# Optimization experiments

Hardware: AMD Instinct MI355X
Metric: run time of the kernel (lower is better)

## Reference

```python
import jax, jax.numpy as jnp
import numpy as np

B, S, D, H = 4, 4096, 1024, 128

def setup_inputs() -> dict:
    key = jax.random.key(0)
    ks = jax.random.split(key, 4)
    scale = 1.0 / np.sqrt(D)
    return {
        "x":  jax.random.normal(ks[0], (B, S, D), dtype=jnp.float32),
        "Wq": jax.random.normal(ks[1], (D, H), dtype=jnp.float32) * scale,
        "bq": jnp.zeros((H,), dtype=jnp.float32),
        "Wk": jax.random.normal(ks[2], (D, H), dtype=jnp.float32) * scale,
        "bk": jnp.zeros((H,), dtype=jnp.float32),
        "Wv": jax.random.normal(ks[3], (D, H), dtype=jnp.float32) * scale,
        "bv": jnp.zeros((H,), dtype=jnp.float32),
    }

def reference(x, Wq, bq, Wk, bk, Wv, bv):
    # q, k, v: [B, S, H]
    q = x @ Wq + bq
    k = x @ Wk + bk
    v = x @ Wv + bv
    inv_sqrt_h = 1.0 / jnp.sqrt(jnp.asarray(q.shape[-1], q.dtype))
    # scores: [B, S, S]
    scores = jnp.einsum('bqh,bkh->bqk', q, k) * inv_sqrt_h
    seq = q.shape[1]
    causal = jnp.tril(jnp.ones((seq, seq), dtype=bool))
    scores = jnp.where(causal, scores, jnp.asarray(-jnp.inf, scores.dtype))
    probs = jax.nn.softmax(scores, axis=-1)
    # dropout p=0.0 -> identity
    return jnp.einsum('bqk,bkh->bqh', probs, v)
```

## Files before the change

### kernel.cpp

```cpp
#include <hip/hip_runtime.h>
#include <hip/hip_bf16.h>

#define B_ 4
#define S_ 4096
#define D_ 1024
#define H_ 128

typedef _Float16 half8 __attribute__((ext_vector_type(8)));
typedef _Float16 half4v __attribute__((ext_vector_type(4)));
typedef float float4v __attribute__((ext_vector_type(4)));


__global__ __launch_bounds__(256) void k_cvt_w(const float* __restrict__ Wq,
                                               const float* __restrict__ Wk,
                                               const float* __restrict__ Wv,
                                               _Float16* __restrict__ WT) {
    const float* W = blockIdx.y == 0 ? Wq : (blockIdx.y == 1 ? Wk : Wv);
    int idx = blockIdx.x * 256 + threadIdx.x;
    int k = idx >> 7, n = idx & 127;
    WT[(size_t)blockIdx.y * (H_ * D_) + (size_t)n * D_ + k] = (_Float16)W[idx];
}

__global__ __launch_bounds__(256, 3) void k_proj(const float* __restrict__ X,
                                                 const _Float16* __restrict__ WT,
                                                 const float* __restrict__ bq,
                                                 const float* __restrict__ bk,
                                                 const float* __restrict__ bv,
                                                 _Float16* __restrict__ Qf,
                                                 _Float16* __restrict__ Kz,
                                                 _Float16* __restrict__ Vz) {
    __shared__ _Float16 smem[(64 + 128) * 72];
    _Float16* As = smem;
    _Float16* Bs = smem + 64 * 72;

    const int t    = threadIdx.x;
    const int bid  = blockIdx.x;
    const int w    = bid >> 8;
    const int m0   = (bid & 255) * 64;
    const int lane = t & 63, wid = t >> 6;
    const int lo   = lane & 15, hi = lane >> 4;
    const int wr   = wid >> 1, wc = wid & 1;

    const _Float16* Wt = WT + (size_t)w * (H_ * D_);

    const int ar = t >> 2, ac = (t & 3) * 16;
    const int br = t >> 1, bc = (t & 1) * 32;

    float4v acc[2][4];
#pragma unroll
    for (int mt = 0; mt < 2; ++mt)
#pragma unroll
        for (int nt = 0; nt < 4; ++nt) acc[mt][nt] = {0.f, 0.f, 0.f, 0.f};

    for (int it = 0; it < 16; ++it) {
        const int k0 = it * 64;
        __syncthreads();
        {
            const float* xp = X + (size_t)(m0 + ar) * D_ + k0 + ac;
            float4v x0 = *(const float4v*)(xp);
            float4v x1 = *(const float4v*)(xp + 4);
            float4v x2 = *(const float4v*)(xp + 8);
            float4v x3 = *(const float4v*)(xp + 12);
            half8 h0, h1;
            h0[0]=(_Float16)x0[0]; h0[1]=(_Float16)x0[1]; h0[2]=(_Float16)x0[2]; h0[3]=(_Float16)x0[3];
            h0[4]=(_Float16)x1[0]; h0[5]=(_Float16)x1[1]; h0[6]=(_Float16)x1[2]; h0[7]=(_Float16)x1[3];
            h1[0]=(_Float16)x2[0]; h1[1]=(_Float16)x2[1]; h1[2]=(_Float16)x2[2]; h1[3]=(_Float16)x2[3];
            h1[4]=(_Float16)x3[0]; h1[5]=(_Float16)x3[1]; h1[6]=(_Float16)x3[2]; h1[7]=(_Float16)x3[3];
            *(half8*)(&As[ar * 72 + ac])     = h0;
            *(half8*)(&As[ar * 72 + ac + 8]) = h1;
        }
        {
            const _Float16* wp = Wt + (size_t)br * D_ + k0 + bc;
            half8 b0 = *(const half8*)(wp);
            half8 b1 = *(const half8*)(wp + 8);
            half8 b2 = *(const half8*)(wp + 16);
            half8 b3 = *(const half8*)(wp + 24);
            *(half8*)(&Bs[br * 72 + bc])      = b0;
            *(half8*)(&Bs[br * 72 + bc + 8])  = b1;
            *(half8*)(&Bs[br * 72 + bc + 16]) = b2;
            *(half8*)(&Bs[br * 72 + bc + 24]) = b3;
        }
        __syncthreads();
#pragma unroll
        for (int kk = 0; kk < 2; ++kk) {
            half8 af[2], bf[4];
#pragma unroll
            for (int mt = 0; mt < 2; ++mt)
                af[mt] = *(const half8*)(&As[(wr * 32 + mt * 16 + lo) * 72 + kk * 32 + hi * 8]);
#pragma unroll
            for (int nt = 0; nt < 4; ++nt)
                bf[nt] = *(const half8*)(&Bs[(wc * 64 + nt * 16 + lo) * 72 + kk * 32 + hi * 8]);
#pragma unroll
            for (int mt = 0; mt < 2; ++mt)
#pragma unroll
                for (int nt = 0; nt < 4; ++nt)
                    acc[mt][nt] = __builtin_amdgcn_mfma_f32_16x16x32_f16(
                        af[mt], bf[nt], acc[mt][nt], 0, 0, 0);
        }
    }

    const float* bias = (w == 0) ? bq : ((w == 1) ? bk : bv);
    const float scale = (w == 0) ? (0.08838834764831845f * 1.4426950408889634f) : 1.0f;
    __syncthreads();
    _Float16* Ct = smem;
#pragma unroll
    for (int mt = 0; mt < 2; ++mt)
#pragma unroll
        for (int nt = 0; nt < 4; ++nt) {
            const int col   = wc * 64 + nt * 16 + lo;
            const float bn  = bias[col];
            const int rbase = wr * 32 + mt * 16 + 4 * hi;
#pragma unroll
            for (int j = 0; j < 4; ++j)
                Ct[(rbase + j) * 136 + col] = (_Float16)((acc[mt][nt][j] + bn) * scale);
        }
    __syncthreads();

    const int bb  = m0 >> 12;
    const int tt0 = (m0 & (S_ - 1)) >> 5;

    if (w == 0) {
        const int r = t >> 2, c0 = (t & 3) * 32;
        _Float16* dst = Qf + (size_t)(m0 + r) * H_ + c0;
        const _Float16* srcp = &Ct[r * 136 + c0];
#pragma unroll
        for (int cc = 0; cc < 4; ++cc)
            *(half8*)(dst + cc * 8) = *(const half8*)(srcp + cc * 8);
    } else if (w == 1) {
        const int rowp = ((lo >> 2) << 3) + (lo & 3);
#pragma unroll
        for (int q = 0; q < 4; ++q) {
            const int fid = wid * 4 + q;
            const int ft = fid >> 3, k2 = (fid >> 1) & 3, c = fid & 1;
            const int row = ft * 32 + rowp + 4 * c;
            half8 v = *(const half8*)(&Ct[row * 136 + k2 * 32 + hi * 8]);
            *(half8*)(Kz + (size_t)(bb * 128 + tt0 + ft) * 4096 +
                      (k2 * 2 + c) * 512 + lane * 8) = v;
        }
    } else {
#pragma unroll
        for (int q = 0; q < 4; ++q) {
            const int fid = wid * 4 + q;
            const int ft = fid >> 3, hc = fid & 7;
            half8 v;
#pragma unroll
            for (int e = 0; e < 8; ++e)
                v[e] = Ct[(ft * 32 + hi * 8 + e) * 136 + hc * 16 + lo];
            *(half8*)(Vz + (size_t)(bb * 128 + tt0 + ft) * 4096 +
                      hc * 512 + lane * 8) = v;
        }
    }
}

__global__ __launch_bounds__(512, 2) void k_attn(const _Float16* __restrict__ Qf,
                                                 const _Float16* __restrict__ Kz,
                                                 const _Float16* __restrict__ Vz,
                                                 float* __restrict__ Out) {
    __shared__ float    sm_l[8][32];
    __shared__ _Float16 sm_o[8][32][136];

    const int t    = threadIdx.x;
    const int lane = t & 63, wid = t >> 6;
    const int lo = lane & 15, hi = lane >> 4;

    const int i   = blockIdx.x;
    const int b   = (i >> 1) & 3;
    const int qtr = ((i >> 3) << 1) | (i & 1);
    const int qt  = (qtr < 64) ? qtr : (191 - qtr);
    const int q0  = qt << 5;

    const _Float16* Qb = Qf + (size_t)b * (S_ * H_);
    const _Float16* Kb = Kz + (size_t)b * 524288;
    const _Float16* Vb = Vz + (size_t)b * 524288;

    half8 qfa[4], qfb[4];
#pragma unroll
    for (int kk = 0; kk < 4; ++kk) {
        qfa[kk] = *(const half8*)(Qb + (size_t)(q0 + lo) * H_ + kk * 32 + hi * 8);
        qfb[kk] = *(const half8*)(Qb + (size_t)(q0 + 16 + lo) * H_ + kk * 32 + hi * 8);
    }

    float4v oa[8], ob[8];
#pragma unroll
    for (int hc = 0; hc < 8; ++hc) { oa[hc] = {0.f,0.f,0.f,0.f}; ob[hc] = {0.f,0.f,0.f,0.f}; }
    float la = 0.f, lb = 0.f;

    const int lane8 = lane * 8;
    const int ntiles = qt + 1;

    half8 kc0[4], kc1[4];
    if (wid < ntiles) {
        const _Float16* Kt = Kb + (size_t)wid * 4096 + lane8;
#pragma unroll
        for (int kk = 0; kk < 4; ++kk) {
            kc0[kk] = *(const half8*)(Kt + (kk * 2    ) * 512);
            kc1[kk] = *(const half8*)(Kt + (kk * 2 + 1) * 512);
        }
    }

    for (int tt = wid; tt < ntiles; tt += 8) {
        const _Float16* Vt = Vb + (size_t)tt * 4096 + lane8;
        half8 vf[8];
#pragma unroll
        for (int hc = 0; hc < 8; ++hc)
            vf[hc] = *(const half8*)(Vt + hc * 512);
        const int tn = (tt + 8 < ntiles) ? (tt + 8) : tt;
        half8 kn0[4], kn1[4];
        {
            const _Float16* Ktn = Kb + (size_t)tn * 4096 + lane8;
#pragma unroll
            for (int kk = 0; kk < 4; ++kk) {
                kn0[kk] = *(const half8*)(Ktn + (kk * 2    ) * 512);
                kn1[kk] = *(const half8*)(Ktn + (kk * 2 + 1) * 512);
            }
        }
        float4v s0a = {0.f,0.f,0.f,0.f}, s1a = {0.f,0.f,0.f,0.f};
        float4v s0b = {0.f,0.f,0.f,0.f}, s1b = {0.f,0.f,0.f,0.f};
#pragma unroll
        for (int kk = 0; kk < 4; ++kk) {
            s0a = __builtin_amdgcn_mfma_f32_16x16x32_f16(kc0[kk], qfa[kk], s0a, 0, 0, 0);
            s0b = __builtin_amdgcn_mfma_f32_16x16x32_f16(kc0[kk], qfb[kk], s0b, 0, 0, 0);
            s1a = __builtin_amdgcn_mfma_f32_16x16x32_f16(kc1[kk], qfa[kk], s1a, 0, 0, 0);
            s1b = __builtin_amdgcn_mfma_f32_16x16x32_f16(kc1[kk], qfb[kk], s1b, 0, 0, 0);
        }
        if (tt == qt) {
#pragma unroll
            for (int j = 0; j < 4; ++j) {
                const int c0 = 8 * hi + j, c1 = 8 * hi + 4 + j;
                if (c0 > lo)      s0a[j] = -INFINITY;
                if (c1 > lo)      s1a[j] = -INFINITY;
                if (c0 > 16 + lo) s0b[j] = -INFINITY;
                if (c1 > 16 + lo) s1b[j] = -INFINITY;
            }
        }
        float pa0 = __builtin_amdgcn_exp2f(s0a[0]), pa1 = __builtin_amdgcn_exp2f(s0a[1]);
        float pa2 = __builtin_amdgcn_exp2f(s0a[2]), pa3 = __builtin_amdgcn_exp2f(s0a[3]);
        float pa4 = __builtin_amdgcn_exp2f(s1a[0]), pa5 = __builtin_amdgcn_exp2f(s1a[1]);
        float pa6 = __builtin_amdgcn_exp2f(s1a[2]), pa7 = __builtin_amdgcn_exp2f(s1a[3]);
        float pb0 = __builtin_amdgcn_exp2f(s0b[0]), pb1 = __builtin_amdgcn_exp2f(s0b[1]);
        float pb2 = __builtin_amdgcn_exp2f(s0b[2]), pb3 = __builtin_amdgcn_exp2f(s0b[3]);
        float pb4 = __builtin_amdgcn_exp2f(s1b[0]), pb5 = __builtin_amdgcn_exp2f(s1b[1]);
        float pb6 = __builtin_amdgcn_exp2f(s1b[2]), pb7 = __builtin_amdgcn_exp2f(s1b[3]);
        la += ((pa0+pa1)+(pa2+pa3)) + ((pa4+pa5)+(pa6+pa7));
        lb += ((pb0+pb1)+(pb2+pb3)) + ((pb4+pb5)+(pb6+pb7));
        half8 pfa, pfb;
        pfa[0]=(_Float16)pa0; pfa[1]=(_Float16)pa1; pfa[2]=(_Float16)pa2; pfa[3]=(_Float16)pa3;
        pfa[4]=(_Float16)pa4; pfa[5]=(_Float16)pa5; pfa[6]=(_Float16)pa6; pfa[7]=(_Float16)pa7;
        pfb[0]=(_Float16)pb0; pfb[1]=(_Float16)pb1; pfb[2]=(_Float16)pb2; pfb[3]=(_Float16)pb3;
        pfb[4]=(_Float16)pb4; pfb[5]=(_Float16)pb5; pfb[6]=(_Float16)pb6; pfb[7]=(_Float16)pb7;
#pragma unroll
        for (int hc = 0; hc < 8; ++hc) {
            oa[hc] = __builtin_amdgcn_mfma_f32_16x16x32_f16(vf[hc], pfa, oa[hc], 0, 0, 0);
            ob[hc] = __builtin_amdgcn_mfma_f32_16x16x32_f16(vf[hc], pfb, ob[hc], 0, 0, 0);
        }
#pragma unroll
        for (int kk = 0; kk < 4; ++kk) { kc0[kk] = kn0[kk]; kc1[kk] = kn1[kk]; }
    }

    la += __shfl_xor(la, 16); la += __shfl_xor(la, 32);
    lb += __shfl_xor(lb, 16); lb += __shfl_xor(lb, 32);

    sm_l[wid][lo]      = la;
    sm_l[wid][16 + lo] = lb;
#pragma unroll
    for (int hc = 0; hc < 8; ++hc) {
        half4v va, vb;
#pragma unroll
        for (int j = 0; j < 4; ++j) { va[j] = (_Float16)oa[hc][j]; vb[j] = (_Float16)ob[hc][j]; }
        *(half4v*)(&sm_o[wid][lo][hc * 16 + 4 * hi])      = va;
        *(half4v*)(&sm_o[wid][16 + lo][hc * 16 + 4 * hi]) = vb;
    }
    __syncthreads();

#pragma unroll
    for (int qh = 0; qh < 2; ++qh) {
        const int q = qh * 16 + lo;
        float L = 0.f;
#pragma unroll
        for (int w = 0; w < 8; ++w) L += sm_l[w][q];
        const float invL = 1.f / L;
        float4v ov = {0.f, 0.f, 0.f, 0.f};
#pragma unroll
        for (int w = 0; w < 8; ++w) {
            half4v tv = *(const half4v*)(&sm_o[w][q][wid * 16 + 4 * hi]);
#pragma unroll
            for (int j = 0; j < 4; ++j) ov[j] += (float)tv[j];
        }
#pragma unroll
        for (int j = 0; j < 4; ++j) ov[j] *= invL;
        *(float4v*)(Out + ((size_t)b * S_ + q0 + q) * H_ + wid * 16 + 4 * hi) = ov;
    }
}

extern "C" void kernel_launch(void* const* d_in, const int* in_sizes, int n_in,
                              void* d_out, int out_size, void* d_ws, size_t ws_size,
                              hipStream_t stream) {
    const float* x  = (const float*)d_in[0];
    const float* Wq = (const float*)d_in[1];
    const float* bq = (const float*)d_in[2];
    const float* Wk = (const float*)d_in[3];
    const float* bk = (const float*)d_in[4];
    const float* Wv = (const float*)d_in[5];
    const float* bv = (const float*)d_in[6];
    float* out = (float*)d_out;

    char* ws = (char*)d_ws;
    _Float16* WT = (_Float16*)ws;
    _Float16* Qf = (_Float16*)(ws + 786432);
    _Float16* Kz = (_Float16*)(ws + 786432 + 4194304);
    _Float16* Vz = (_Float16*)(ws + 786432 + 8388608);

    hipLaunchKernelGGL(k_cvt_w, dim3(512, 3), dim3(256), 0, stream, Wq, Wk, Wv, WT);
    hipLaunchKernelGGL(k_proj, dim3(768), dim3(256), 0, stream,
                       x, WT, bq, bk, bv, Qf, Kz, Vz);
    hipLaunchKernelGGL(k_attn, dim3(512), dim3(512), 0, stream, Qf, Kz, Vz, out);
}
```

Measured before the change: 68.17 us.

## Prefetch projection tiles into registers and double K-tile depth

The QKV projection GEMM now issues global loads for the next K tile into registers before computing on the current tile held in shared memory, so memory latency can overlap the MFMA work. The K tile grows from 64 to 128, which halves the number of loop iterations and barriers. The global load mapping changes to row-strided float4/half8 accesses that coalesce better. In exchange it uses more registers and LDS per block (about 51KB), which may reduce occupancy below the launch-bounds target of 3 blocks.

```diff
diff --git a/kernel.cpp b/kernel.cpp
--- a/kernel.cpp
+++ b/kernel.cpp
@@ -29,9 +29,9 @@
                                                  _Float16* __restrict__ Qf,
                                                  _Float16* __restrict__ Kz,
                                                  _Float16* __restrict__ Vz) {
-    __shared__ _Float16 smem[(64 + 128) * 72];
+    __shared__ _Float16 smem[64 * 136 + 128 * 136];
     _Float16* As = smem;
-    _Float16* Bs = smem + 64 * 72;
+    _Float16* Bs = smem + 64 * 136;
 
     const int t    = threadIdx.x;
     const int bid  = blockIdx.x;
@@ -43,8 +43,17 @@
 
     const _Float16* Wt = WT + (size_t)w * (H_ * D_);
 
-    const int ar = t >> 2, ac = (t & 3) * 16;
-    const int br = t >> 1, bc = (t & 1) * 32;
+    const int xr = t >> 5, xc = (t & 31) * 4;
+    const int br = t >> 4, bc = (t & 15) * 8;
+
+    float4v xreg[8];
+    half8   wreg[8];
+#pragma unroll
+    for (int i2 = 0; i2 < 8; ++i2)
+        xreg[i2] = *(const float4v*)(X + (size_t)(m0 + xr + i2 * 8) * D_ + xc);
+#pragma unroll
+    for (int i2 = 0; i2 < 8; ++i2)
+        wreg[i2] = *(const half8*)(Wt + (size_t)(br + i2 * 16) * D_ + bc);
 
     float4v acc[2][4];
 #pragma unroll
@@ -52,44 +61,38 @@
 #pragma unroll
         for (int nt = 0; nt < 4; ++nt) acc[mt][nt] = {0.f, 0.f, 0.f, 0.f};
 
-    for (int it = 0; it < 16; ++it) {
-        const int k0 = it * 64;
+    for (int it = 0; it < 8; ++it) {
         __syncthreads();
-        {
-            const float* xp = X + (size_t)(m0 + ar) * D_ + k0 + ac;
-            float4v x0 = *(const float4v*)(xp);
-            float4v x1 = *(const float4v*)(xp + 4);
-            float4v x2 = *(const float4v*)(xp + 8);
-            float4v x3 = *(const float4v*)(xp + 12);
-            half8 h0, h1;
-            h0[0]=(_Float16)x0[0]; h0[1]=(_Float16)x0[1]; h0[2]=(_Float16)x0[2]; h0[3]=(_Float16)x0[3];
-            h0[4]=(_Float16)x1[0]; h0[5]=(_Float16)x1[1]; h0[6]=(_Float16)x1[2]; h0[7]=(_Float16)x1[3];
-            h1[0]=(_Float16)x2[0]; h1[1]=(_Float16)x2[1]; h1[2]=(_Float16)x2[2]; h1[3]=(_Float16)x2[3];
-            h1[4]=(_Float16)x3[0]; h1[5]=(_Float16)x3[1]; h1[6]=(_Float16)x3[2]; h1[7]=(_Float16)x3[3];
-            *(half8*)(&As[ar * 72 + ac])     = h0;
-            *(half8*)(&As[ar * 72 + ac + 8]) = h1;
-        }
-        {
-            const _Float16* wp = Wt + (size_t)br * D_ + k0 + bc;
-            half8 b0 = *(const half8*)(wp);
-            half8 b1 = *(const half8*)(wp + 8);
-            half8 b2 = *(const half8*)(wp + 16);
-            half8 b3 = *(const half8*)(wp + 24);
-            *(half8*)(&Bs[br * 72 + bc])      = b0;
-            *(half8*)(&Bs[br * 72 + bc + 8])  = b1;
-            *(half8*)(&Bs[br * 72 + bc + 16]) = b2;
-            *(half8*)(&Bs[br * 72 + bc + 24]) = b3;
+#pragma unroll
+        for (int i2 = 0; i2 < 8; ++i2) {
+            float4v xv = xreg[i2];
+            half4v hv;
+            hv[0] = (_Float16)xv[0]; hv[1] = (_Float16)xv[1];
+            hv[2] = (_Float16)xv[2]; hv[3] = (_Float16)xv[3];
+            *(half4v*)(&As[(xr + i2 * 8) * 136 + xc]) = hv;
+        }
+#pragma unroll
+        for (int i2 = 0; i2 < 8; ++i2)
+            *(half8*)(&Bs[(br + i2 * 16) * 136 + bc]) = wreg[i2];
+        if (it < 7) {
+            const int k0n = (it + 1) * 128;
+#pragma unroll
+            for (int i2 = 0; i2 < 8; ++i2)
+                xreg[i2] = *(const float4v*)(X + (size_t)(m0 + xr + i2 * 8) * D_ + k0n + xc);
+#pragma unroll
+            for (int i2 = 0; i2 < 8; ++i2)
+                wreg[i2] = *(const half8*)(Wt + (size_t)(br + i2 * 16) * D_ + k0n + bc);
         }
         __syncthreads();
 #pragma unroll
-        for (int kk = 0; kk < 2; ++kk) {
+        for (int kk = 0; kk < 4; ++kk) {
             half8 af[2], bf[4];
 #pragma unroll
             for (int mt = 0; mt < 2; ++mt)
-                af[mt] = *(const half8*)(&As[(wr * 32 + mt * 16 + lo) * 72 + kk * 32 + hi * 8]);
+                af[mt] = *(const half8*)(&As[(wr * 32 + mt * 16 + lo) * 136 + kk * 32 + hi * 8]);
 #pragma unroll
             for (int nt = 0; nt < 4; ++nt)
-                bf[nt] = *(const half8*)(&Bs[(wc * 64 + nt * 16 + lo) * 72 + kk * 32 + hi * 8]);
+                bf[nt] = *(const half8*)(&Bs[(wc * 64 + nt * 16 + lo) * 136 + kk * 32 + hi * 8]);
 #pragma unroll
             for (int mt = 0; mt < 2; ++mt)
 #pragma unroll
```

Result: no change. 68.03 us (-0.2%).

## Load projection MFMA fragments directly from global memory with pre-swizzled weights

Applied to the files above, without the earlier changes.

The weight conversion kernel now writes the fp16 weights in MFMA fragment order, so each lane can load its B operand with one contiguous half8 read. The projection kernel drops shared-memory staging and barriers in its K loop, reads X directly from global memory into registers and converts it there, and doubles the tile to 128 rows, with half as many blocks and occupancy lowered to 2. The aim is to remove LDS traffic and synchronisation. In exchange X loads are strided per lane rather than coalesced through LDS, and there are fewer blocks for the GPU's many CUs.

```diff
diff --git a/kernel.cpp b/kernel.cpp
--- a/kernel.cpp
+++ b/kernel.cpp
@@ -14,102 +14,80 @@
 __global__ __launch_bounds__(256) void k_cvt_w(const float* __restrict__ Wq,
                                                const float* __restrict__ Wk,
                                                const float* __restrict__ Wv,
-                                               _Float16* __restrict__ WT) {
+                                               _Float16* __restrict__ WTz) {
     const float* W = blockIdx.y == 0 ? Wq : (blockIdx.y == 1 ? Wk : Wv);
-    int idx = blockIdx.x * 256 + threadIdx.x;
-    int k = idx >> 7, n = idx & 127;
-    WT[(size_t)blockIdx.y * (H_ * D_) + (size_t)n * D_ + k] = (_Float16)W[idx];
-}
-
-__global__ __launch_bounds__(256, 3) void k_proj(const float* __restrict__ X,
-                                                 const _Float16* __restrict__ WT,
+    const int idx  = blockIdx.x * 256 + threadIdx.x;
+    const int lane = idx & 63, ntg = (idx >> 6) & 7, K32 = idx >> 9;
+    const int lo = lane & 15, hi = lane >> 4;
+    half8 v;
+#pragma unroll
+    for (int e = 0; e < 8; ++e)
+        v[e] = (_Float16)W[(K32 * 32 + hi * 8 + e) * H_ + ntg * 16 + lo];
+    *(half8*)(WTz + (size_t)(((int)blockIdx.y * 32 + K32) * 8 + ntg) * 512 + lane * 8) = v;
+}
+
+__global__ __launch_bounds__(256, 2) void k_proj(const float* __restrict__ X,
+                                                 const _Float16* __restrict__ WTz,
                                                  const float* __restrict__ bq,
                                                  const float* __restrict__ bk,
                                                  const float* __restrict__ bv,
                                                  _Float16* __restrict__ Qf,
                                                  _Float16* __restrict__ Kz,
                                                  _Float16* __restrict__ Vz) {
-    __shared__ _Float16 smem[(64 + 128) * 72];
-    _Float16* As = smem;
-    _Float16* Bs = smem + 64 * 72;
-
-    const int t    = threadIdx.x;
-    const int bid  = blockIdx.x;
-    const int w    = bid >> 8;
-    const int m0   = (bid & 255) * 64;
-    const int lane = t & 63, wid = t >> 6;
-    const int lo   = lane & 15, hi = lane >> 4;
-    const int wr   = wid >> 1, wc = wid & 1;
-
-    const _Float16* Wt = WT + (size_t)w * (H_ * D_);
-
-    const int ar = t >> 2, ac = (t & 3) * 16;
-    const int br = t >> 1, bc = (t & 1) * 32;
-
-    float4v acc[2][4];
-#pragma unroll
-    for (int mt = 0; mt < 2; ++mt)
+    __shared__ _Float16 Ct[128 * 136];
+
+    const int t     = threadIdx.x;
+    const int bid   = blockIdx.x;
+    const int w     = bid >> 7;
+    const int panel = bid & 127;
+    const int m0    = panel * 128;
+    const int lane  = t & 63, wid = t >> 6;
+    const int lo    = lane & 15, hi = lane >> 4;
+    const int wr    = wid >> 1, wc = wid & 1;
+
+    const float*    Xw = X + (size_t)(m0 + wr * 64 + lo) * D_ + hi * 8;
+    const _Float16* Bw = WTz + (size_t)(w * 32 * 8 + wc * 4) * 512 + lane * 8;
+
+    float4v acc[4][4];
+#pragma unroll
+    for (int mt = 0; mt < 4; ++mt)
 #pragma unroll
         for (int nt = 0; nt < 4; ++nt) acc[mt][nt] = {0.f, 0.f, 0.f, 0.f};
 
-    for (int it = 0; it < 16; ++it) {
-        const int k0 = it * 64;
-        __syncthreads();
-        {
-            const float* xp = X + (size_t)(m0 + ar) * D_ + k0 + ac;
+#pragma unroll 4
+    for (int K32 = 0; K32 < 32; ++K32) {
+        half8 bf[4];
+#pragma unroll
+        for (int nt = 0; nt < 4; ++nt)
+            bf[nt] = *(const half8*)(Bw + (size_t)(K32 * 8 + nt) * 512);
+        half8 af[4];
+#pragma unroll
+        for (int mt = 0; mt < 4; ++mt) {
+            const float* xp = Xw + (size_t)mt * 16 * D_ + K32 * 32;
             float4v x0 = *(const float4v*)(xp);
             float4v x1 = *(const float4v*)(xp + 4);
-            float4v x2 = *(const float4v*)(xp + 8);
-            float4v x3 = *(const float4v*)(xp + 12);
-            half8 h0, h1;
-            h0[0]=(_Float16)x0[0]; h0[1]=(_Float16)x0[1]; h0[2]=(_Float16)x0[2]; h0[3]=(_Float16)x0[3];
-            h0[4]=(_Float16)x1[0]; h0[5]=(_Float16)x1[1]; h0[6]=(_Float16)x1[2]; h0[7]=(_Float16)x1[3];
-            h1[0]=(_Float16)x2[0]; h1[1]=(_Float16)x2[1]; h1[2]=(_Float16)x2[2]; h1[3]=(_Float16)x2[3];
-            h1[4]=(_Float16)x3[0]; h1[5]=(_Float16)x3[1]; h1[6]=(_Float16)x3[2]; h1[7]=(_Float16)x3[3];
-            *(half8*)(&As[ar * 72 + ac])     = h0;
-            *(half8*)(&As[ar * 72 + ac + 8]) = h1;
-        }
-        {
-            const _Float16* wp = Wt + (size_t)br * D_ + k0 + bc;
-            half8 b0 = *(const half8*)(wp);
-            half8 b1 = *(const half8*)(wp + 8);
-            half8 b2 = *(const half8*)(wp + 16);
-            half8 b3 = *(const half8*)(wp + 24);
-            *(half8*)(&Bs[br * 72 + bc])      = b0;
-            *(half8*)(&Bs[br * 72 + bc + 8])  = b1;
-            *(half8*)(&Bs[br * 72 + bc + 16]) = b2;
-            *(half8*)(&Bs[br * 72 + bc + 24]) = b3;
-        }
-        __syncthreads();
-#pragma unroll
-        for (int kk = 0; kk < 2; ++kk) {
-            half8 af[2], bf[4];
-#pragma unroll
-            for (int mt = 0; mt < 2; ++mt)
-                af[mt] = *(const half8*)(&As[(wr * 32 + mt * 16 + lo) * 72 + kk * 32 + hi * 8]);
+            half8 h;
+            h[0]=(_Float16)x0[0]; h[1]=(_Float16)x0[1]; h[2]=(_Float16)x0[2]; h[3]=(_Float16)x0[3];
+            h[4]=(_Float16)x1[0]; h[5]=(_Float16)x1[1]; h[6]=(_Float16)x1[2]; h[7]=(_Float16)x1[3];
+            af[mt] = h;
+        }
+#pragma unroll
+        for (int mt = 0; mt < 4; ++mt)
 #pragma unroll
             for (int nt = 0; nt < 4; ++nt)
-                bf[nt] = *(const half8*)(&Bs[(wc * 64 + nt * 16 + lo) * 72 + kk * 32 + hi * 8]);
-#pragma unroll
-            for (int mt = 0; mt < 2; ++mt)
-#pragma unroll
-                for (int nt = 0; nt < 4; ++nt)
-                    acc[mt][nt] = __builtin_amdgcn_mfma_f32_16x16x32_f16(
-                        af[mt], bf[nt], acc[mt][nt], 0, 0, 0);
-        }
+                acc[mt][nt] = __builtin_amdgcn_mfma_f32_16x16x32_f16(
+                    af[mt], bf[nt], acc[mt][nt], 0, 0, 0);
     }
 
     const float* bias = (w == 0) ? bq : ((w == 1) ? bk : bv);
     const float scale = (w == 0) ? (0.08838834764831845f * 1.4426950408889634f) : 1.0f;
-    __syncthreads();
-    _Float16* Ct = smem;
-#pragma unroll
-    for (int mt = 0; mt < 2; ++mt)
+#pragma unroll
+    for (int mt = 0; mt < 4; ++mt)
 #pragma unroll
         for (int nt = 0; nt < 4; ++nt) {
             const int col   = wc * 64 + nt * 16 + lo;
             const float bn  = bias[col];
-            const int rbase = wr * 32 + mt * 16 + 4 * hi;
+            const int rbase = wr * 64 + mt * 16 + 4 * hi;
 #pragma unroll
             for (int j = 0; j < 4; ++j)
                 Ct[(rbase + j) * 136 + col] = (_Float16)((acc[mt][nt][j] + bn) * scale);
@@ -120,17 +98,17 @@
     const int tt0 = (m0 & (S_ - 1)) >> 5;
 
     if (w == 0) {
-        const int r = t >> 2, c0 = (t & 3) * 32;
+        const int r = t >> 1, c0 = (t & 1) * 64;
         _Float16* dst = Qf + (size_t)(m0 + r) * H_ + c0;
         const _Float16* srcp = &Ct[r * 136 + c0];
 #pragma unroll
-        for (int cc = 0; cc < 4; ++cc)
+        for (int cc = 0; cc < 8; ++cc)
             *(half8*)(dst + cc * 8) = *(const half8*)(srcp + cc * 8);
     } else if (w == 1) {
         const int rowp = ((lo >> 2) << 3) + (lo & 3);
 #pragma unroll
-        for (int q = 0; q < 4; ++q) {
-            const int fid = wid * 4 + q;
+        for (int q = 0; q < 8; ++q) {
+            const int fid = wid * 8 + q;
             const int ft = fid >> 3, k2 = (fid >> 1) & 3, c = fid & 1;
             const int row = ft * 32 + rowp + 4 * c;
             half8 v = *(const half8*)(&Ct[row * 136 + k2 * 32 + hi * 8]);
@@ -139,8 +117,8 @@
         }
     } else {
 #pragma unroll
-        for (int q = 0; q < 4; ++q) {
-            const int fid = wid * 4 + q;
+        for (int q = 0; q < 8; ++q) {
+            const int fid = wid * 8 + q;
             const int ft = fid >> 3, hc = fid & 7;
             half8 v;
 #pragma unroll
@@ -305,13 +283,13 @@
     float* out = (float*)d_out;
 
     char* ws = (char*)d_ws;
-    _Float16* WT = (_Float16*)ws;
-    _Float16* Qf = (_Float16*)(ws + 786432);
-    _Float16* Kz = (_Float16*)(ws + 786432 + 4194304);
-    _Float16* Vz = (_Float16*)(ws + 786432 + 8388608);
-
-    hipLaunchKernelGGL(k_cvt_w, dim3(512, 3), dim3(256), 0, stream, Wq, Wk, Wv, WT);
-    hipLaunchKernelGGL(k_proj, dim3(768), dim3(256), 0, stream,
-                       x, WT, bq, bk, bv, Qf, Kz, Vz);
+    _Float16* WTz = (_Float16*)ws;
+    _Float16* Qf  = (_Float16*)(ws + 786432);
+    _Float16* Kz  = (_Float16*)(ws + 786432 + 4194304);
+    _Float16* Vz  = (_Float16*)(ws + 786432 + 8388608);
+
+    hipLaunchKernelGGL(k_cvt_w, dim3(64, 3), dim3(256), 0, stream, Wq, Wk, Wv, WTz);
+    hipLaunchKernelGGL(k_proj, dim3(384), dim3(256), 0, stream,
+                       x, WTz, bq, bk, bv, Qf, Kz, Vz);
     hipLaunchKernelGGL(k_attn, dim3(512), dim3(512), 0, stream, Qf, Kz, Vz, out);
 }
```

New measurement: 106.2 us. +55.8%, slower.

## Load projection tiles directly into LDS with swizzled global_load_lds

Applied to the files above, without the earlier changes.

The projection GEMM now stages X (kept as fp32) and the fp16 weight tiles into LDS using direct global-to-LDS loads, bypassing registers. It uses an XOR swizzle in place of padding to avoid bank conflicts. The fp32-to-fp16 conversion of X moves to after the LDS read, so the X tile in LDS doubles in size and each element is converted once per consuming wave. The aim is fewer registers and less VALU work in the load path, which may let loads overlap better. The cost is more LDS traffic and repeated conversions.

```diff
diff --git a/kernel.cpp b/kernel.cpp
--- a/kernel.cpp
+++ b/kernel.cpp
@@ -10,6 +10,12 @@
 typedef _Float16 half4v __attribute__((ext_vector_type(4)));
 typedef float float4v __attribute__((ext_vector_type(4)));
 
+
+__device__ __forceinline__ void gload_lds16(const void* g, void* l) {
+    __builtin_amdgcn_global_load_lds(
+        (const __attribute__((address_space(1))) unsigned int*)g,
+        (__attribute__((address_space(3))) unsigned int*)l, 16, 0, 0);
+}
 
 __global__ __launch_bounds__(256) void k_cvt_w(const float* __restrict__ Wq,
                                                const float* __restrict__ Wk,
@@ -29,9 +35,9 @@
                                                  _Float16* __restrict__ Qf,
                                                  _Float16* __restrict__ Kz,
                                                  _Float16* __restrict__ Vz) {
-    __shared__ _Float16 smem[(64 + 128) * 72];
-    _Float16* As = smem;
-    _Float16* Bs = smem + 64 * 72;
+    __shared__ char smem[32768];
+    char* AsB = smem;
+    char* BsB = smem + 16384;
 
     const int t    = threadIdx.x;
     const int bid  = blockIdx.x;
@@ -43,8 +49,10 @@
 
     const _Float16* Wt = WT + (size_t)w * (H_ * D_);
 
-    const int ar = t >> 2, ac = (t & 3) * 16;
-    const int br = t >> 1, bc = (t & 1) * 32;
+    const int raj = wid * 16 + (lane >> 4);
+    const int rbj = wid * 32 + (lane >> 3);
+    const int ca0 = (lane & 15) * 4;
+    const int cb0 = (lane & 7) * 8;
 
     float4v acc[2][4];
 #pragma unroll
@@ -54,42 +62,40 @@
 
     for (int it = 0; it < 16; ++it) {
         const int k0 = it * 64;
+#pragma unroll
+        for (int j = 0; j < 4; ++j) {
+            const int ra = raj + j * 4;
+            const int ca = ca0 ^ ((ra & 7) * 4);
+            gload_lds16(X + (size_t)(m0 + ra) * D_ + k0 + ca,
+                        AsB + (wid * 16 + j * 4) * 256);
+            const int rb = rbj + j * 8;
+            const int cb = cb0 ^ ((rb & 7) * 8);
+            gload_lds16(Wt + (size_t)rb * D_ + k0 + cb,
+                        BsB + (wid * 32 + j * 8) * 128);
+        }
         __syncthreads();
-        {
-            const float* xp = X + (size_t)(m0 + ar) * D_ + k0 + ac;
-            float4v x0 = *(const float4v*)(xp);
-            float4v x1 = *(const float4v*)(xp + 4);
-            float4v x2 = *(const float4v*)(xp + 8);
-            float4v x3 = *(const float4v*)(xp + 12);
-            half8 h0, h1;
-            h0[0]=(_Float16)x0[0]; h0[1]=(_Float16)x0[1]; h0[2]=(_Float16)x0[2]; h0[3]=(_Float16)x0[3];
-            h0[4]=(_Float16)x1[0]; h0[5]=(_Float16)x1[1]; h0[6]=(_Float16)x1[2]; h0[7]=(_Float16)x1[3];
-            h1[0]=(_Float16)x2[0]; h1[1]=(_Float16)x2[1]; h1[2]=(_Float16)x2[2]; h1[3]=(_Float16)x2[3];
-            h1[4]=(_Float16)x3[0]; h1[5]=(_Float16)x3[1]; h1[6]=(_Float16)x3[2]; h1[7]=(_Float16)x3[3];
-            *(half8*)(&As[ar * 72 + ac])     = h0;
-            *(half8*)(&As[ar * 72 + ac + 8]) = h1;
-        }
-        {
-            const _Float16* wp = Wt + (size_t)br * D_ + k0 + bc;
-            half8 b0 = *(const half8*)(wp);
-            half8 b1 = *(const half8*)(wp + 8);
-            half8 b2 = *(const half8*)(wp + 16);
-            half8 b3 = *(const half8*)(wp + 24);
-            *(half8*)(&Bs[br * 72 + bc])      = b0;
-            *(half8*)(&Bs[br * 72 + bc + 8])  = b1;
-            *(half8*)(&Bs[br * 72 + bc + 16]) = b2;
-            *(half8*)(&Bs[br * 72 + bc + 24]) = b3;
-        }
-        __syncthreads();
 #pragma unroll
         for (int kk = 0; kk < 2; ++kk) {
-            half8 af[2], bf[4];
-#pragma unroll
-            for (int mt = 0; mt < 2; ++mt)
-                af[mt] = *(const half8*)(&As[(wr * 32 + mt * 16 + lo) * 72 + kk * 32 + hi * 8]);
-#pragma unroll
-            for (int nt = 0; nt < 4; ++nt)
-                bf[nt] = *(const half8*)(&Bs[(wc * 64 + nt * 16 + lo) * 72 + kk * 32 + hi * 8]);
+            const int cb = kk * 32 + hi * 8;
+            half8 af[2];
+#pragma unroll
+            for (int mt = 0; mt < 2; ++mt) {
+                const int r = wr * 32 + mt * 16 + lo;
+                const int v = (r & 7) * 4;
+                float4v a0 = *(const float4v*)(AsB + r * 256 + ((cb ^ v) << 2));
+                float4v a1 = *(const float4v*)(AsB + r * 256 + (((cb + 4) ^ v) << 2));
+                half8 h;
+                h[0]=(_Float16)a0[0]; h[1]=(_Float16)a0[1]; h[2]=(_Float16)a0[2]; h[3]=(_Float16)a0[3];
+                h[4]=(_Float16)a1[0]; h[5]=(_Float16)a1[1]; h[6]=(_Float16)a1[2]; h[7]=(_Float16)a1[3];
+                af[mt] = h;
+            }
+            half8 bf[4];
+#pragma unroll
+            for (int nt = 0; nt < 4; ++nt) {
+                const int rb2 = wc * 64 + nt * 16 + lo;
+                const int vb  = (rb2 & 7) * 8;
+                bf[nt] = *(const half8*)(BsB + rb2 * 128 + (((cb) ^ vb) << 1));
+            }
 #pragma unroll
             for (int mt = 0; mt < 2; ++mt)
 #pragma unroll
@@ -97,12 +103,12 @@
                     acc[mt][nt] = __builtin_amdgcn_mfma_f32_16x16x32_f16(
                         af[mt], bf[nt], acc[mt][nt], 0, 0, 0);
         }
+        __syncthreads();
     }
 
     const float* bias = (w == 0) ? bq : ((w == 1) ? bk : bv);
     const float scale = (w == 0) ? (0.08838834764831845f * 1.4426950408889634f) : 1.0f;
-    __syncthreads();
-    _Float16* Ct = smem;
+    _Float16* Ct = (_Float16*)smem;
 #pragma unroll
     for (int mt = 0; mt < 2; ++mt)
 #pragma unroll
```

Result: faster. 60.44 us (-11.3%).
